# Optimization experiments

Hardware: AMD Instinct MI355X
Metric: run time of the kernel (lower is better)

The kernel has to match this reference:

```python
import jax, jax.numpy as jnp
import numpy as np
from jax import lax

WIN = 7            # win_size
K = 0.03           # stability constant
COV_NORM = WIN * WIN / (WIN * WIN - 1.0)  # faithful: win_size**2 / (win_size**2 - 1)


def setup_inputs() -> dict:
    key = jax.random.key(0)
    kx, ky = jax.random.split(key)
    x = jax.random.normal(kx, (2, 4, 160, 160, 96), dtype=jnp.float32)
    y = jax.random.randint(ky, (2, 1, 160, 160, 96), 0, 4, dtype=jnp.int64)
    return {"x": x, "y": y}


def _box_mean(a):
    s = lax.reduce_window(a, jnp.array(0, a.dtype), lax.add,
                          (1, 1, WIN, WIN, WIN), (1, 1, 1, 1, 1), 'VALID')
    return s / jnp.asarray(WIN ** 3, a.dtype)


def reference(x, y):
    B, C, H, W, D = x.shape
    # one_hot(y, num_classes=C): (B,1,H,W,D) int -> (B,C,H,W,D) float
    y1 = jnp.moveaxis(jax.nn.one_hot(y[:, 0], C, dtype=x.dtype), -1, 1)
    xr = x.reshape(-1, 1, H, W, D)
    yr = y1.reshape(-1, 1, H, W, D)
    xr = xr * yr
    data_range = jnp.max(yr)
    xr = jax.nn.sigmoid(xr)
    c = (K * data_range) ** 2 / 2
    ux = _box_mean(xr)
    uy = _box_mean(yr)
    uxx = _box_mean(xr * xr)
    uyy = _box_mean(yr * yr)
    uxy = _box_mean(xr * yr)
    vx = COV_NORM * (uxx - ux * ux)
    vy = COV_NORM * (uyy - uy * uy)
    vxy = COV_NORM * (uxy - ux * uy)
    s_value = (vxy + c) / (vx * vy + c)
    return 1.0 - jnp.mean(s_value)
```

## Files before the change

### kernel.cpp

```cpp
#include <hip/hip_runtime.h>
#include <hip/hip_fp16.h>

#define WINS 7
#define H 160
#define W 160
#define DD 96
#define HO 154
#define WO 154
#define DOUT 90
#define CSTRIDE (H*W*DD)

#define TH 8
#define TW 8
#define TD 24
#define IH 14
#define IW 14
#define NCOL (IH * IW)
#define IDS 32
#define IDW 30
#define NDP 15
#define SAS 30
#define SBC 49
#define HTILES 20
#define WTILES 20
#define DTILES 4


struct alignas(8) Half4 { __half x, y, z, w; };

static __device__ __forceinline__ __half2 u2h(unsigned int a) {
    __half2 r; __builtin_memcpy(&r, &a, 4); return r;
}
static __device__ __forceinline__ unsigned int h2u(__half2 v) {
    unsigned int r; __builtin_memcpy(&r, &v, 4); return r;
}
static __device__ __forceinline__ void pmask(__half2 v, __half2& p, __half2& m) {
    const unsigned int bits = h2u(v);
    const unsigned int neg  = bits & 0x80008000u;
    const unsigned int full = (neg >> 15) * 0xFFFFu;
    p = u2h(bits & ~full);
    m = u2h(((~bits >> 15) & 0x00010001u) * 0x3C00u);
}

__device__ __forceinline__ float sval(float c0, float c1, float c2) {
    const float S_t  = c1 + 0.5f  * (343.0f - c0);
    const float S_t2 = c2 + 0.25f * (343.0f - c0);
    const float inv  = 1.0f / 343.0f;
    const float ux   = S_t  * inv;
    const float uy   = c0   * inv;
    const float uxx  = S_t2 * inv;
    const float uxy  = c1   * inv;
    const float covn = 49.0f / 48.0f;
    const float cc   = 0.00045f;
    const float vx  = covn * (uxx - ux * ux);
    const float vy  = covn * (uy  - uy * uy);
    const float vxy = covn * (uxy - ux * uy);
    return (vxy + cc) * __builtin_amdgcn_rcpf(vx * vy + cc);
}

__global__ __launch_bounds__(256)
void sigmoid_prepass(const float* __restrict__ x,
                     const int* __restrict__ y,
                     __half* __restrict__ xs,
                     double* __restrict__ acc) {
    if (blockIdx.x == 0 && blockIdx.y == 0 && threadIdx.x == 0) acc[0] = 0.0;
    const int b  = blockIdx.y;
    const int qv = blockIdx.x * 256 + threadIdx.x;
    const int off = 4 * qv;
    const int4 yv = *(const int4*)(y + (size_t)b * CSTRIDE + off);
#pragma unroll
    for (int c = 0; c < 4; c++) {
        const size_t xo = ((size_t)(b * 4 + c)) * CSTRIDE + off;
        const float4 xv = *(const float4*)(x + xo);
        const float s0 = 1.0f / (1.0f + __expf(-xv.x));
        const float s1 = 1.0f / (1.0f + __expf(-xv.y));
        const float s2 = 1.0f / (1.0f + __expf(-xv.z));
        const float s3 = 1.0f / (1.0f + __expf(-xv.w));
        Half4 hv;
        hv.x = __float2half((yv.x == c) ? s0 : -s0);
        hv.y = __float2half((yv.y == c) ? s1 : -s1);
        hv.z = __float2half((yv.z == c) ? s2 : -s2);
        hv.w = __float2half((yv.w == c) ? s3 : -s3);
        *(Half4*)(xs + xo) = hv;
    }
}

template <bool PRE>
__global__ __launch_bounds__(256, 5)
void structure_loss_main(const float* __restrict__ x,
                         const int* __restrict__ y,
                         const __half* __restrict__ xs,
                         double* __restrict__ acc) {
    __shared__ __half sA0[IH * TW * SAS];
    __shared__ __half sA1[IH * TW * SAS];
    __shared__ __half sA2[IH * TW * SAS];
    __shared__ union alignas(16) {
        __half  vs[NCOL * IDS];
        __half2 sb2[64 * SBC + 3];
    } u;
    __shared__ unsigned int yb[PRE ? 1 : NCOL * 2];
    __shared__ float wsum[4];

    const int dt = blockIdx.x;
    const int wt = blockIdx.y;
    const int z  = blockIdx.z;
    const int b  = z / HTILES;
    const int ht = z - b * HTILES;

    const int h0 = ht * TH, w0 = wt * TW;
    const int d0 = dt * TD;
    const int dstage = (dt == DTILES - 1) ? 64 : d0;
    const int doff = d0 - dstage;
    const int odmax = min(TD, DOUT - d0);
    const int* yc = y + (size_t)b * (size_t)CSTRIDE;
    const int t = threadIdx.x;

    if (!PRE) {
        for (int i = t; i < NCOL * 2; i += 256) {
            const int col = i >> 1, hf = i & 1;
            const int ih = col / IW, iw = col - ih * IW;
            const int h = min(h0 + ih, H - 1);
            const int w = min(w0 + iw, W - 1);
            const size_t cb = (size_t)(h * W + w) * DD;
            const int dstart = dstage + 16 * hf;
            unsigned int pk = 0u;
#pragma unroll
            for (int j3 = 0; j3 < 4; j3++) {
                const int4 yv = *(const int4*)(yc + cb + dstart + 4 * j3);
                pk |= (unsigned)(yv.x & 3) << (2 * (4 * j3 + 0));
                pk |= (unsigned)(yv.y & 3) << (2 * (4 * j3 + 1));
                pk |= (unsigned)(yv.z & 3) << (2 * (4 * j3 + 2));
                pk |= (unsigned)(yv.w & 3) << (2 * (4 * j3 + 3));
            }
            yb[i] = pk;
        }
        __syncthreads();
    }

    float lsum = 0.f;

    for (int cl = 0; cl < 4; cl++) {
        if (PRE) {
            const __half* xsc = xs + ((size_t)b * 4 + cl) * (size_t)CSTRIDE;
#pragma unroll
            for (int k = 0; k < 4; k++) {
                const int i = t + 256 * k;
                if (i < NCOL * 4) {
                    const int col = i >> 2, q = i & 3;
                    const int ih = col / IW, iw = col - ih * IW;
                    const int h = min(h0 + ih, H - 1);
                    const int w = min(w0 + iw, W - 1);
                    const uint4 vv =
                        *(const uint4*)(xsc + (h * W + w) * DD + dstage + 8 * q);
                    *(uint4*)&u.vs[col * IDS + 8 * q] = vv;
                }
            }
        } else {
            const float* xc = x + ((size_t)b * 4 + cl) * (size_t)CSTRIDE;
#pragma unroll
            for (int k = 0; k < 7; k++) {
                const int i = t + 256 * k;
                if (i < NCOL * 8) {
                    const int col = i >> 3, q = i & 7;
                    const int ih = col / IW, iw = col - ih * IW;
                    const int h = min(h0 + ih, H - 1);
                    const int w = min(w0 + iw, W - 1);
                    const int dbase = dstage + 4 * q;
                    const float4 xv = *(const float4*)(xc + (h * W + w) * DD + dbase);
                    const unsigned int pk = yb[col * 2 + (q >> 2)] >> (8 * (q & 3));
                    const float s0 = 1.0f / (1.0f + __expf(-xv.x));
                    const float s1 = 1.0f / (1.0f + __expf(-xv.y));
                    const float s2 = 1.0f / (1.0f + __expf(-xv.z));
                    const float s3 = 1.0f / (1.0f + __expf(-xv.w));
                    Half4 hv;
                    hv.x = __float2half(((int)((pk >> 0) & 3u) == cl) ? s0 : -s0);
                    hv.y = __float2half(((int)((pk >> 2) & 3u) == cl) ? s1 : -s1);
                    hv.z = __float2half(((int)((pk >> 4) & 3u) == cl) ? s2 : -s2);
                    hv.w = __float2half(((int)((pk >> 6) & 3u) == cl) ? s3 : -s3);
                    *(Half4*)&u.vs[col * IDS + 4 * q] = hv;
                }
            }
        }
        __syncthreads();

        if (t < IH * NDP) {
            const int ih = t / NDP, dp = t - ih * NDP;
            const int s  = min(doff + 2 * dp, IDS - 2);
            const __half2 z2 = __float2half2_rn(0.f);
            __half2 v2[IW];
            const int vbase = ih * IW * IDS + s;
#pragma unroll
            for (int iw = 0; iw < IW; iw++)
                v2[iw] = *(const __half2*)&u.vs[vbase + iw * IDS];
            __half2 sm = z2, sp = z2, sq = z2;
#pragma unroll
            for (int iw = 0; iw < WINS; iw++) {
                __half2 p, m;
                pmask(v2[iw], p, m);
                sm = __hadd2(sm, m);
                sp = __hadd2(sp, p);
                sq = __hfma2(p, v2[iw], sq);
            }
            int o = (ih * TW) * SAS + 2 * dp;
            *(__half2*)&sA0[o] = sm;
            *(__half2*)&sA1[o] = sp;
            *(__half2*)&sA2[o] = sq;
#pragma unroll
            for (int wo = 1; wo < TW; wo++) {
                const __half2 a = v2[wo + 6], bb = v2[wo - 1];
                __half2 pa, ma, pb, mb;
                pmask(a, pa, ma);
                pmask(bb, pb, mb);
                sm = __hadd2(sm, __hsub2(ma, mb));
                sp = __hadd2(sp, __hsub2(pa, pb));
                sq = __hadd2(sq, __hsub2(__hmul2(pa, a), __hmul2(pb, bb)));
                o += SAS;
                *(__half2*)&sA0[o] = sm;
                *(__half2*)&sA1[o] = sp;
                *(__half2*)&sA2[o] = sq;
            }
        }
        __syncthreads();

        if (t < 2 * TW * NDP) {
            const int dp = t % NDP;
            const int r  = t / NDP;
            const int wo = r & 7;
            const int ho0 = (r >> 3) * 4;
            __half2 a0[10], a1[10], a2[10];
#pragma unroll
            for (int k = 0; k < 10; k++) {
                const int idx = ((ho0 + k) * TW + wo) * SAS + 2 * dp;
                a0[k] = *(const __half2*)&sA0[idx];
                a1[k] = *(const __half2*)&sA1[idx];
                a2[k] = *(const __half2*)&sA2[idx];
            }
            __half2 s0 = a0[0], s1 = a1[0], s2 = a2[0];
#pragma unroll
            for (int k = 1; k < WINS; k++) {
                s0 = __hadd2(s0, a0[k]);
                s1 = __hadd2(s1, a1[k]);
                s2 = __hadd2(s2, a2[k]);
            }
            int o = ((ho0 * TW + wo) * SBC) + dp * 3;
            u.sb2[o] = s0; u.sb2[o + 1] = s1; u.sb2[o + 2] = s2;
#pragma unroll
            for (int k = 1; k < 4; k++) {
                s0 = __hadd2(s0, __hsub2(a0[k + 6], a0[k - 1]));
                s1 = __hadd2(s1, __hsub2(a1[k + 6], a1[k - 1]));
                s2 = __hadd2(s2, __hsub2(a2[k + 6], a2[k - 1]));
                o += TW * SBC;
                u.sb2[o] = s0; u.sb2[o + 1] = s1; u.sb2[o + 2] = s2;
            }
        }
        __syncthreads();

        {
            const int dq = t & 3;
            const int wo = (t >> 2) & 7;
            const int ho = t >> 5;
            const int hg = h0 + ho, wg = w0 + wo;
            if (hg < HO && wg < WO) {
                const int base2 = (ho * TW + wo) * SBC + 9 * dq;
                float b0[12], b1[12], b2[12];
#pragma unroll
                for (int k = 0; k < 6; k++) {
                    float2 f;
                    f = __half22float2(u.sb2[base2 + 3 * k + 0]);
                    b0[2 * k] = f.x; b0[2 * k + 1] = f.y;
                    f = __half22float2(u.sb2[base2 + 3 * k + 1]);
                    b1[2 * k] = f.x; b1[2 * k + 1] = f.y;
                    f = __half22float2(u.sb2[base2 + 3 * k + 2]);
                    b2[2 * k] = f.x; b2[2 * k + 1] = f.y;
                }
                float s0 = 0.f, s1 = 0.f, s2 = 0.f;
#pragma unroll
                for (int k = 0; k < WINS; k++) { s0 += b0[k]; s1 += b1[k]; s2 += b2[k]; }
                const int od0 = 6 * dq;
#pragma unroll
                for (int k = 0; k < 6; k++) {
                    if (k > 0) {
                        s0 += b0[k + 6] - b0[k - 1];
                        s1 += b1[k + 6] - b1[k - 1];
                        s2 += b2[k + 6] - b2[k - 1];
                    }
                    if (od0 + k < odmax) lsum += sval(s0, s1, s2);
                }
            }
        }
        __syncthreads();
    }

#pragma unroll
    for (int off = 32; off > 0; off >>= 1) lsum += __shfl_down(lsum, off, 64);
    const int wave = t >> 6;
    if ((t & 63) == 0) wsum[wave] = lsum;
    __syncthreads();
    if (t == 0) {
        const float s = wsum[0] + wsum[1] + wsum[2] + wsum[3];
        atomicAdd(acc, (double)s);
    }
}

__global__ void structure_loss_finalize(const double* __restrict__ acc,
                                        float* __restrict__ out) {
    out[0] = 1.0f - (float)(acc[0] / 17075520.0);
}

extern "C" void kernel_launch(void* const* d_in, const int* in_sizes, int n_in,
                              void* d_out, int out_size, void* d_ws, size_t ws_size,
                              hipStream_t stream) {
    const float* x = (const float*)d_in[0];
    const int*   y = (const int*)d_in[1];
    double* acc = (double*)d_ws;
    __half* xs = (__half*)((char*)d_ws + 16);

    const size_t need = 16 + (size_t)8 * CSTRIDE * sizeof(__half);
    dim3 grid(DTILES, WTILES, 2 * HTILES);

    if (ws_size >= need) {
        sigmoid_prepass<<<dim3(2400, 2), 256, 0, stream>>>(x, y, xs, acc);
        structure_loss_main<true><<<grid, 256, 0, stream>>>(x, y, xs, acc);
    } else {
        (void)hipMemsetAsync(d_ws, 0, sizeof(double), stream);
        structure_loss_main<false><<<grid, 256, 0, stream>>>(x, y, xs, acc);
    }
    structure_loss_finalize<<<1, 1, 0, stream>>>(acc, (float*)d_out);
}
```

Measured before the change: 199.3 us.

## Load precomputed half values directly from global in W-pass, drop staging sync

In the precomputed-input path, the W-direction pass now reads its half2 values straight from global memory with precomputed clamped offsets, instead of first staging a tile in shared memory and synchronising. The vs/sb2 shared union is split into separate buffers so the trailing barrier at the end of each class iteration can be removed. Per-thread index math is hoisted out of the class loop. This trades coalesced vector staging loads for strided 4-byte global loads, and the extra shared memory may reduce occupancy.

```diff
diff --git a/kernel.cpp b/kernel.cpp
--- a/kernel.cpp
+++ b/kernel.cpp
@@ -17,7 +17,6 @@
 #define IW 14
 #define NCOL (IH * IW)
 #define IDS 32
-#define IDW 30
 #define NDP 15
 #define SAS 30
 #define SBC 49
@@ -94,10 +93,8 @@
     __shared__ __half sA0[IH * TW * SAS];
     __shared__ __half sA1[IH * TW * SAS];
     __shared__ __half sA2[IH * TW * SAS];
-    __shared__ union alignas(16) {
-        __half  vs[NCOL * IDS];
-        __half2 sb2[64 * SBC + 3];
-    } u;
+    __shared__ __half2 sb2[64 * SBC + 3];
+    __shared__ __half vsF[PRE ? 2 : NCOL * IDS];
     __shared__ unsigned int yb[PRE ? 1 : NCOL * 2];
     __shared__ float wsum[4];
 
@@ -114,6 +111,52 @@
     const int odmax = min(TD, DOUT - d0);
     const int* yc = y + (size_t)b * (size_t)CSTRIDE;
     const int t = threadIdx.x;
+
+    const bool actA = (t < IH * NDP);
+    const int  ihA  = t / NDP, dpA = t - ihA * NDP;
+    const int  sA_  = min(doff + 2 * dpA, IDS - 2);
+    const int  hA   = min(h0 + ihA, H - 1);
+    const int  wmax = min(IW - 1, W - 1 - w0);
+    const int  gb0  = (hA * W + w0) * DD + dstage + sA_;
+    int goff[IW];
+#pragma unroll
+    for (int iw = 0; iw < IW; iw++) goff[iw] = gb0 + min(iw, wmax) * DD;
+    const int  oA0  = (ihA * TW) * SAS + 2 * dpA;
+    const bool actB = (t < 2 * TW * NDP);
+    const int  rB   = t / NDP, dpB = t - rB * NDP;
+    const int  woB  = rB & 7, ho0B = (rB >> 3) * 4;
+    const int  idxB0 = (ho0B * TW + woB) * SAS + 2 * dpB;
+    const int  oB0   = (ho0B * TW + woB) * SBC + dpB * 3;
+    const int  dqC  = t & 3, woC = (t >> 2) & 7, hoC = t >> 5;
+    const bool actC = (h0 + hoC < HO) && (w0 + woC < WO);
+    const int  base2C = (hoC * TW + woC) * SBC + 9 * dqC;
+
+    auto stageF = [&](int cc) {
+        const float* xc = x + ((size_t)b * 4 + cc) * (size_t)CSTRIDE;
+#pragma unroll
+        for (int k = 0; k < 7; k++) {
+            const int i = t + 256 * k;
+            if (i < NCOL * 8) {
+                const int col = i >> 3, q = i & 7;
+                const int ih = col / IW, iw = col - ih * IW;
+                const int h = min(h0 + ih, H - 1);
+                const int w = min(w0 + iw, W - 1);
+                const int dbase = dstage + 4 * q;
+                const float4 xv = *(const float4*)(xc + (h * W + w) * DD + dbase);
+                const unsigned int pk = yb[col * 2 + (q >> 2)] >> (8 * (q & 3));
+                const float s0 = 1.0f / (1.0f + __expf(-xv.x));
+                const float s1 = 1.0f / (1.0f + __expf(-xv.y));
+                const float s2 = 1.0f / (1.0f + __expf(-xv.z));
+                const float s3 = 1.0f / (1.0f + __expf(-xv.w));
+                Half4 hv;
+                hv.x = __float2half(((int)((pk >> 0) & 3u) == cc) ? s0 : -s0);
+                hv.y = __float2half(((int)((pk >> 2) & 3u) == cc) ? s1 : -s1);
+                hv.z = __float2half(((int)((pk >> 4) & 3u) == cc) ? s2 : -s2);
+                hv.w = __float2half(((int)((pk >> 6) & 3u) == cc) ? s3 : -s3);
+                *(Half4*)&vsF[col * IDS + 4 * q] = hv;
+            }
+        }
+    };
 
     if (!PRE) {
         for (int i = t; i < NCOL * 2; i += 256) {
@@ -140,58 +183,24 @@
     float lsum = 0.f;
 
     for (int cl = 0; cl < 4; cl++) {
-        if (PRE) {
-            const __half* xsc = xs + ((size_t)b * 4 + cl) * (size_t)CSTRIDE;
-#pragma unroll
-            for (int k = 0; k < 4; k++) {
-                const int i = t + 256 * k;
-                if (i < NCOL * 4) {
-                    const int col = i >> 2, q = i & 3;
-                    const int ih = col / IW, iw = col - ih * IW;
-                    const int h = min(h0 + ih, H - 1);
-                    const int w = min(w0 + iw, W - 1);
-                    const uint4 vv =
-                        *(const uint4*)(xsc + (h * W + w) * DD + dstage + 8 * q);
-                    *(uint4*)&u.vs[col * IDS + 8 * q] = vv;
-                }
-            }
-        } else {
-            const float* xc = x + ((size_t)b * 4 + cl) * (size_t)CSTRIDE;
-#pragma unroll
-            for (int k = 0; k < 7; k++) {
-                const int i = t + 256 * k;
-                if (i < NCOL * 8) {
-                    const int col = i >> 3, q = i & 7;
-                    const int ih = col / IW, iw = col - ih * IW;
-                    const int h = min(h0 + ih, H - 1);
-                    const int w = min(w0 + iw, W - 1);
-                    const int dbase = dstage + 4 * q;
-                    const float4 xv = *(const float4*)(xc + (h * W + w) * DD + dbase);
-                    const unsigned int pk = yb[col * 2 + (q >> 2)] >> (8 * (q & 3));
-                    const float s0 = 1.0f / (1.0f + __expf(-xv.x));
-                    const float s1 = 1.0f / (1.0f + __expf(-xv.y));
-                    const float s2 = 1.0f / (1.0f + __expf(-xv.z));
-                    const float s3 = 1.0f / (1.0f + __expf(-xv.w));
-                    Half4 hv;
-                    hv.x = __float2half(((int)((pk >> 0) & 3u) == cl) ? s0 : -s0);
-                    hv.y = __float2half(((int)((pk >> 2) & 3u) == cl) ? s1 : -s1);
-                    hv.z = __float2half(((int)((pk >> 4) & 3u) == cl) ? s2 : -s2);
-                    hv.w = __float2half(((int)((pk >> 6) & 3u) == cl) ? s3 : -s3);
-                    *(Half4*)&u.vs[col * IDS + 4 * q] = hv;
-                }
-            }
-        }
-        __syncthreads();
-
-        if (t < IH * NDP) {
-            const int ih = t / NDP, dp = t - ih * NDP;
-            const int s  = min(doff + 2 * dp, IDS - 2);
+        if (!PRE) {
+            stageF(cl);
+            __syncthreads();
+        }
+
+        if (actA) {
+            __half2 v2[IW];
+            if (PRE) {
+                const __half* xcl = xs + (size_t)(4 * b + cl) * (size_t)CSTRIDE;
+#pragma unroll
+                for (int iw = 0; iw < IW; iw++)
+                    v2[iw] = *(const __half2*)(xcl + goff[iw]);
+            } else {
+#pragma unroll
+                for (int iw = 0; iw < IW; iw++)
+                    v2[iw] = *(const __half2*)&vsF[(ihA * IW + iw) * IDS + sA_];
+            }
             const __half2 z2 = __float2half2_rn(0.f);
-            __half2 v2[IW];
-            const int vbase = ih * IW * IDS + s;
-#pragma unroll
-            for (int iw = 0; iw < IW; iw++)
-                v2[iw] = *(const __half2*)&u.vs[vbase + iw * IDS];
             __half2 sm = z2, sp = z2, sq = z2;
 #pragma unroll
             for (int iw = 0; iw < WINS; iw++) {
@@ -201,7 +210,7 @@
                 sp = __hadd2(sp, p);
                 sq = __hfma2(p, v2[iw], sq);
             }
-            int o = (ih * TW) * SAS + 2 * dp;
+            int o = oA0;
             *(__half2*)&sA0[o] = sm;
             *(__half2*)&sA1[o] = sp;
             *(__half2*)&sA2[o] = sq;
@@ -222,15 +231,11 @@
         }
         __syncthreads();
 
-        if (t < 2 * TW * NDP) {
-            const int dp = t % NDP;
-            const int r  = t / NDP;
-            const int wo = r & 7;
-            const int ho0 = (r >> 3) * 4;
+        if (actB) {
             __half2 a0[10], a1[10], a2[10];
 #pragma unroll
             for (int k = 0; k < 10; k++) {
-                const int idx = ((ho0 + k) * TW + wo) * SAS + 2 * dp;
+                const int idx = idxB0 + k * (TW * SAS);
                 a0[k] = *(const __half2*)&sA0[idx];
                 a1[k] = *(const __half2*)&sA1[idx];
                 a2[k] = *(const __half2*)&sA2[idx];
@@ -242,53 +247,45 @@
                 s1 = __hadd2(s1, a1[k]);
                 s2 = __hadd2(s2, a2[k]);
             }
-            int o = ((ho0 * TW + wo) * SBC) + dp * 3;
-            u.sb2[o] = s0; u.sb2[o + 1] = s1; u.sb2[o + 2] = s2;
+            int o = oB0;
+            sb2[o] = s0; sb2[o + 1] = s1; sb2[o + 2] = s2;
 #pragma unroll
             for (int k = 1; k < 4; k++) {
                 s0 = __hadd2(s0, __hsub2(a0[k + 6], a0[k - 1]));
                 s1 = __hadd2(s1, __hsub2(a1[k + 6], a1[k - 1]));
                 s2 = __hadd2(s2, __hsub2(a2[k + 6], a2[k - 1]));
                 o += TW * SBC;
-                u.sb2[o] = s0; u.sb2[o + 1] = s1; u.sb2[o + 2] = s2;
+                sb2[o] = s0; sb2[o + 1] = s1; sb2[o + 2] = s2;
             }
         }
         __syncthreads();
 
-        {
-            const int dq = t & 3;
-            const int wo = (t >> 2) & 7;
-            const int ho = t >> 5;
-            const int hg = h0 + ho, wg = w0 + wo;
-            if (hg < HO && wg < WO) {
-                const int base2 = (ho * TW + wo) * SBC + 9 * dq;
-                float b0[12], b1[12], b2[12];
-#pragma unroll
-                for (int k = 0; k < 6; k++) {
-                    float2 f;
-                    f = __half22float2(u.sb2[base2 + 3 * k + 0]);
-                    b0[2 * k] = f.x; b0[2 * k + 1] = f.y;
-                    f = __half22float2(u.sb2[base2 + 3 * k + 1]);
-                    b1[2 * k] = f.x; b1[2 * k + 1] = f.y;
-                    f = __half22float2(u.sb2[base2 + 3 * k + 2]);
-                    b2[2 * k] = f.x; b2[2 * k + 1] = f.y;
+        if (actC) {
+            float b0[12], b1[12], b2[12];
+#pragma unroll
+            for (int k = 0; k < 6; k++) {
+                float2 f;
+                f = __half22float2(sb2[base2C + 3 * k + 0]);
+                b0[2 * k] = f.x; b0[2 * k + 1] = f.y;
+                f = __half22float2(sb2[base2C + 3 * k + 1]);
+                b1[2 * k] = f.x; b1[2 * k + 1] = f.y;
+                f = __half22float2(sb2[base2C + 3 * k + 2]);
+                b2[2 * k] = f.x; b2[2 * k + 1] = f.y;
+            }
+            float s0 = 0.f, s1 = 0.f, s2 = 0.f;
+#pragma unroll
+            for (int k = 0; k < WINS; k++) { s0 += b0[k]; s1 += b1[k]; s2 += b2[k]; }
+            const int od0 = 6 * dqC;
+#pragma unroll
+            for (int k = 0; k < 6; k++) {
+                if (k > 0) {
+                    s0 += b0[k + 6] - b0[k - 1];
+                    s1 += b1[k + 6] - b1[k - 1];
+                    s2 += b2[k + 6] - b2[k - 1];
                 }
-                float s0 = 0.f, s1 = 0.f, s2 = 0.f;
-#pragma unroll
-                for (int k = 0; k < WINS; k++) { s0 += b0[k]; s1 += b1[k]; s2 += b2[k]; }
-                const int od0 = 6 * dq;
-#pragma unroll
-                for (int k = 0; k < 6; k++) {
-                    if (k > 0) {
-                        s0 += b0[k + 6] - b0[k - 1];
-                        s1 += b1[k + 6] - b1[k - 1];
-                        s2 += b2[k + 6] - b2[k - 1];
-                    }
-                    if (od0 + k < odmax) lsum += sval(s0, s1, s2);
-                }
-            }
-        }
-        __syncthreads();
+                if (od0 + k < odmax) lsum += sval(s0, s1, s2);
+            }
+        }
     }
 
 #pragma unroll
```

After: 186.9 us. 6.2% less time.
